# Optimization experiments

Hardware: AMD Instinct MI355X
Metric: run time of the kernel (lower is better)

The kernel has to match this reference:

```python
import jax, jax.numpy as jnp
import numpy as np

D_MODEL = 1024
N_HEADS = 16
D_K = D_MODEL // N_HEADS
B, T = 2, 2048


def setup_inputs() -> dict:
    key = jax.random.key(0)
    ks = jax.random.split(key, 12)
    s = 0.02
    return {
        "q": jax.random.normal(ks[0], (B, T, D_MODEL), jnp.float32),
        "k": jax.random.normal(ks[1], (B, T, D_MODEL), jnp.float32),
        "v": jax.random.normal(ks[2], (B, T, D_MODEL), jnp.float32),
        "Wq": jax.random.normal(ks[3], (D_MODEL, D_MODEL), jnp.float32) * s,
        "bq": jnp.zeros((D_MODEL,), jnp.float32),
        "Wk": jax.random.normal(ks[4], (D_MODEL, D_MODEL), jnp.float32) * s,
        "bk": jnp.zeros((D_MODEL,), jnp.float32),
        "Wv": jax.random.normal(ks[5], (D_MODEL, D_MODEL), jnp.float32) * s,
        "bv": jnp.zeros((D_MODEL,), jnp.float32),
        "Wo": jax.random.normal(ks[6], (D_MODEL, D_MODEL), jnp.float32) * s,
        "bo": jnp.zeros((D_MODEL,), jnp.float32),
        "mask": jnp.ones((B, T), jnp.int32),
        "causal": 1,
    }


def reference(q, k, v, Wq, bq, Wk, bk, Wv, bv, Wo, bo, mask, causal):
    Bq, Tq, D = q.shape
    Tk = k.shape[1]
    # projections (torch Linear: x @ W.T + b), split heads -> [B, H, T, d_k]
    qh = (q @ Wq.T + bq).reshape(Bq, Tq, N_HEADS, D_K).transpose(0, 2, 1, 3)
    kh = (k @ Wk.T + bk).reshape(Bq, Tk, N_HEADS, D_K).transpose(0, 2, 1, 3)
    vh = (v @ Wv.T + bv).reshape(Bq, Tk, N_HEADS, D_K).transpose(0, 2, 1, 3)
    scores = jnp.einsum("bhqd,bhkd->bhqk", qh, kh) / jnp.sqrt(jnp.float32(D_K))
    neg_inf = jnp.float32(-jnp.inf)
    if mask is not None:
        scores = jnp.where(mask[:, None, None, :] == 0, neg_inf, scores)
    if causal:
        causal_mask = jnp.tril(jnp.ones((Tq, Tq), jnp.float32))
        scores = jnp.where(causal_mask == 0, neg_inf, scores)
    attn = jax.nn.softmax(scores, axis=-1)
    out = jnp.einsum("bhqk,bhkd->bhqd", attn, vh)
    out = out.transpose(0, 2, 1, 3).reshape(Bq, Tq, D)
    return out @ Wo.T + bo
```

## Files before the change

kernel.cpp:

```cpp
#include <hip/hip_runtime.h>
#include <cstdint>
#include <cstddef>


typedef __bf16 bf16x8 __attribute__((ext_vector_type(8)));
typedef float f32x4 __attribute__((ext_vector_type(4)));

#define MFMA(a, b, c) __builtin_amdgcn_mfma_f32_16x16x32_bf16((a), (b), (c), 0, 0, 0)

static constexpr int D_MODEL = 1024;
static constexpr int T_ = 2048;
static constexpr int M_TOK = 4096;

__device__ __forceinline__ unsigned short f32_to_bf16(float f) {
    union { float f; uint32_t u; } v; v.f = f;
    uint32_t u = v.u;
    uint32_t r = u + 0x7fffu + ((u >> 16) & 1u);
    return (unsigned short)(r >> 16);
}
__device__ __forceinline__ unsigned f32_to_bf16_fast(float f) {
    union { float f; uint32_t u; } v; v.f = f;
    return (v.u + 0x8000u) >> 16;
}

typedef __attribute__((address_space(1))) void* as1_ptr;
typedef __attribute__((address_space(3))) void* as3_ptr;
__device__ __forceinline__ void gload_lds16(const void* g, void* l) {
    __builtin_amdgcn_global_load_lds((as1_ptr)(void*)g, (as3_ptr)l, 16, 0, 0);
}

__device__ __forceinline__ int keyperm(int k) {
    return (k & 32) | ((k & 12) << 1) | ((k & 16) >> 2) | (k & 3);
}

__global__ __launch_bounds__(256) void cvt_all(
    const float* __restrict__ q, const float* __restrict__ k,
    const float* __restrict__ v, const float* __restrict__ wq,
    const float* __restrict__ wk, const float* __restrict__ wv,
    const float* __restrict__ wo, ushort4* __restrict__ dst) {
    int i = blockIdx.x * blockDim.x + threadIdx.x;
    constexpr int R = 1 << 20;
    const float* s;
    int idx;
    if (i < 3 * R) {
        s = (i < R) ? q : (i < 2 * R) ? k : v;
        idx = i & (R - 1);
    } else {
        int j = i - 3 * R;
        int w = j >> 18;
        s = (w == 0) ? wq : (w == 1) ? wk : (w == 2) ? wv : wo;
        idx = j & ((1 << 18) - 1);
    }
    float4 f = ((const float4*)s)[idx];
    ushort4 o;
    o.x = (unsigned short)f32_to_bf16(f.x); o.y = (unsigned short)f32_to_bf16(f.y);
    o.z = (unsigned short)f32_to_bf16(f.z); o.w = (unsigned short)f32_to_bf16(f.w);
    dst[i] = o;
}

template<int MODE, int NT16>
__device__ __forceinline__ void gemm_body(
    const unsigned short* __restrict__ A, const unsigned short* __restrict__ W,
    const float* __restrict__ bias, void* __restrict__ outp,
    unsigned short* As, unsigned short* Ws, int bx, int by)
{
    constexpr bool SWAP = (MODE != 2);
    constexpr int BKE = 32;
    constexpr int ASZ = 128 * BKE;
    constexpr int WSZ = NT16 * 32 * BKE;
    constexpr int AL = ASZ / (256 * 8);
    constexpr int WL = WSZ / (256 * 8);
    constexpr int NKS = D_MODEL / BKE;
    const int tid = threadIdx.x;
    const int lane = tid & 63, wave = tid >> 6;
    const int wm = wave >> 1, wn = wave & 1;
    const int r16 = lane & 15, kg = lane >> 4;
    const int m_blk = by * 128, n_blk = bx * (NT16 * 32);

    const unsigned short* Ap[AL]; unsigned short* Albase[AL];
    #pragma unroll
    for (int j = 0; j < AL; ++j) {
        int si = j * 256 + tid;
        int row = si >> 2, p = si & 3, g = p ^ ((row >> 1) & 3);
        Ap[j] = A + (size_t)(m_blk + row) * D_MODEL + g * 8;
        Albase[j] = As + (j * 256 + wave * 64) * 8;
    }
    const unsigned short* Wp[WL]; unsigned short* Wlbase[WL];
    #pragma unroll
    for (int j = 0; j < WL; ++j) {
        int si = j * 256 + tid;
        int row = si >> 2, p = si & 3, g = p ^ ((row >> 1) & 3);
        Wp[j] = W + (size_t)(n_blk + row) * D_MODEL + g * 8;
        Wlbase[j] = Ws + (j * 256 + wave * 64) * 8;
    }

    int aoff[4], woff[NT16];
    #pragma unroll
    for (int mt = 0; mt < 4; ++mt) {
        int row = wm * 64 + mt * 16 + r16;
        aoff[mt] = row * BKE + ((kg ^ ((row >> 1) & 3)) * 8);
    }
    #pragma unroll
    for (int nt = 0; nt < NT16; ++nt) {
        int row = wn * (NT16 * 16) + nt * 16 + r16;
        woff[nt] = row * BKE + ((kg ^ ((row >> 1) & 3)) * 8);
    }

    f32x4 acc[4][NT16];
    #pragma unroll
    for (int mt = 0; mt < 4; ++mt)
        #pragma unroll
        for (int nt = 0; nt < NT16; ++nt) acc[mt][nt] = (f32x4){0, 0, 0, 0};

    auto stage = [&](int bb, int k0) {
        #pragma unroll
        for (int j = 0; j < AL; ++j)
            gload_lds16(Ap[j] + k0, Albase[j] + bb * ASZ);
        #pragma unroll
        for (int j = 0; j < WL; ++j)
            gload_lds16(Wp[j] + k0, Wlbase[j] + bb * WSZ);
    };

    stage(0, 0);
    stage(1, BKE);
    int cb = 0;
    for (int ks = 0; ks < NKS; ++ks) {
        if (ks + 1 < NKS) asm volatile("s_waitcnt vmcnt(4)" ::: "memory");
        else              asm volatile("s_waitcnt vmcnt(0)" ::: "memory");
        __builtin_amdgcn_s_barrier();
        __builtin_amdgcn_sched_barrier(0);
        if (ks + 2 < NKS) {
            int sb = cb + 2; if (sb >= 3) sb -= 3;
            stage(sb, (ks + 2) * BKE);
        }
        const unsigned short* Asb = As + cb * ASZ;
        const unsigned short* Wsb = Ws + cb * WSZ;
        bf16x8 af[4], wf[NT16];
        #pragma unroll
        for (int mt = 0; mt < 4; ++mt)
            af[mt] = *(const bf16x8*)(Asb + aoff[mt]);
        #pragma unroll
        for (int nt = 0; nt < NT16; ++nt)
            wf[nt] = *(const bf16x8*)(Wsb + woff[nt]);
        #pragma unroll
        for (int mt = 0; mt < 4; ++mt)
            #pragma unroll
            for (int nt = 0; nt < NT16; ++nt)
                acc[mt][nt] = SWAP ? MFMA(wf[nt], af[mt], acc[mt][nt])
                                   : MFMA(af[mt], wf[nt], acc[mt][nt]);
        cb = (cb == 2) ? 0 : cb + 1;
    }

    if (MODE == 2) {
        #pragma unroll
        for (int nt = 0; nt < NT16; ++nt) {
            int n = n_blk + wn * (NT16 * 16) + nt * 16 + r16;
            float bn = bias[n];
            int hh = n >> 6, dki = n & 63;
            #pragma unroll
            for (int mt = 0; mt < 4; ++mt) {
                int m0 = m_blk + wm * 64 + mt * 16 + kg * 4;
                int mp = (m0 & ~63) | keyperm(m0 & 63);
                int bb = mp >> 11, ti = mp & 2047;
                ushort4 pk;
                pk.x = f32_to_bf16(acc[mt][nt][0] + bn);
                pk.y = f32_to_bf16(acc[mt][nt][1] + bn);
                pk.z = f32_to_bf16(acc[mt][nt][2] + bn);
                pk.w = f32_to_bf16(acc[mt][nt][3] + bn);
                *(ushort4*)((unsigned short*)outp +
                    ((size_t)(bb * 16 + hh) * 64 + dki) * 2048 + ti) = pk;
            }
        }
    } else {
        #pragma unroll
        for (int nt = 0; nt < NT16; ++nt) {
            int n0 = n_blk + wn * (NT16 * 16) + nt * 16 + kg * 4;
            float4 bn4 = *(const float4*)(bias + n0);
            #pragma unroll
            for (int mt = 0; mt < 4; ++mt) {
                int m = m_blk + wm * 64 + mt * 16 + r16;
                if (MODE == 3) {
                    float4 st;
                    st.x = acc[mt][nt][0] + bn4.x; st.y = acc[mt][nt][1] + bn4.y;
                    st.z = acc[mt][nt][2] + bn4.z; st.w = acc[mt][nt][3] + bn4.w;
                    *(float4*)((float*)outp + (size_t)m * D_MODEL + n0) = st;
                } else {
                    ushort4 pk;
                    pk.x = f32_to_bf16(acc[mt][nt][0] + bn4.x);
                    pk.y = f32_to_bf16(acc[mt][nt][1] + bn4.y);
                    pk.z = f32_to_bf16(acc[mt][nt][2] + bn4.z);
                    pk.w = f32_to_bf16(acc[mt][nt][3] + bn4.w);
                    *(ushort4*)((unsigned short*)outp + (size_t)m * D_MODEL + n0) = pk;
                }
            }
        }
    }
}

__global__ __launch_bounds__(256) void gemm_qkv(
    const unsigned short* __restrict__ qb, const unsigned short* __restrict__ kb,
    const unsigned short* __restrict__ vb, const unsigned short* __restrict__ Wqb,
    const unsigned short* __restrict__ Wkb, const unsigned short* __restrict__ Wvb,
    const float* __restrict__ bq, const float* __restrict__ bk, const float* __restrict__ bv,
    unsigned short* __restrict__ Qhp, unsigned short* __restrict__ Khp,
    unsigned short* __restrict__ Vtp)
{
    __shared__ __align__(16) unsigned short As[3 * 128 * 32];
    __shared__ __align__(16) unsigned short Ws[3 * 128 * 32];
    int flat = blockIdx.x + (blockIdx.y << 3) + (blockIdx.z << 8);
    int w = (flat & 7) * 96 + (flat >> 3);
    int bx = w & 7, by = (w >> 3) & 31, z = w >> 8;
    const unsigned short* A = (z == 0) ? qb : (z == 1) ? kb : vb;
    const unsigned short* W = (z == 0) ? Wqb : (z == 1) ? Wkb : Wvb;
    const float* bias = (z == 0) ? bq : (z == 1) ? bk : bv;
    if (z < 2)
        gemm_body<0, 4>(A, W, bias, (z == 0) ? (void*)Qhp : (void*)Khp, As, Ws,
                        bx, by);
    else
        gemm_body<2, 4>(A, W, bias, (void*)Vtp, As, Ws, bx, by);
}

__global__ __launch_bounds__(256) void gemm_out(
    const unsigned short* __restrict__ ab, const unsigned short* __restrict__ Wob,
    const float* __restrict__ bo, float* __restrict__ outp)
{
    __shared__ __align__(16) unsigned short As[3 * 128 * 32];
    __shared__ __align__(16) unsigned short Ws[3 * 128 * 32];
    int flat = blockIdx.x + (blockIdx.y << 3);
    int w = (flat & 7) * 32 + (flat >> 3);
    int bx = w & 7, by = w >> 3;
    gemm_body<3, 4>(ab, Wob, bo, (void*)outp, As, Ws, bx, by);
}

__global__ __launch_bounds__(256) void attn_fwd(
    const unsigned short* __restrict__ Qh, const unsigned short* __restrict__ Kh,
    const unsigned short* __restrict__ Vt, const int* __restrict__ mask,
    const int* __restrict__ causal_p, unsigned short* __restrict__ attnout)
{
    __shared__ __align__(16) unsigned short Ks[2][64 * 64];
    __shared__ __align__(16) unsigned short Vs[2][64 * 64];
    __shared__ unsigned long long kmS[32];

    const int tid = threadIdx.x;
    const int lane = tid & 63, wave = tid >> 6;
    const int bh = blockIdx.x;
    const int y = blockIdx.y, y0 = y & 7, j4 = y >> 3;
    const int qc = (j4 == 0) ? y0 : (j4 == 1) ? (15 - y0)
                 : (j4 == 2) ? (16 + y0) : (31 - y0);
    const int b = bh >> 4, h = bh & 15;
    const int causal = *causal_p;
    const int r16 = lane & 15, kg = lane >> 4;

    const int q0 = qc * 64 + wave * 16;

    const unsigned short* Qb = Qh + (size_t)b * T_ * D_MODEL + h * 64;
    const unsigned short* Kb = Kh + (size_t)b * T_ * D_MODEL + h * 64;
    const unsigned short* Vb = Vt + (size_t)bh * 64 * T_;
    const int* mb = mask + b * T_;

    #pragma unroll
    for (int t = wave; t < 32; t += 4) {
        unsigned long long m = __ballot(mb[t * 64 + lane] != 0);
        if (lane == 0) kmS[t] = m;
    }

    bf16x8 qf0 = *(const bf16x8*)(Qb + (size_t)(q0 + r16) * D_MODEL + kg * 8);
    bf16x8 qf1 = *(const bf16x8*)(Qb + (size_t)(q0 + r16) * D_MODEL + 32 + kg * 8);

    float l = 0.f;
    f32x4 o[4];
    #pragma unroll
    for (int f = 0; f < 4; ++f) o[f] = (f32x4){0, 0, 0, 0};
    const float sc2 = 0.18033688011112042f;
    const int lim = wave * 16 + r16;

    const int nT = causal ? (qc + 1) : 32;

    auto stage = [&](int buf, int t) {
        int t0 = t * 64;
        #pragma unroll
        for (int j = 0; j < 2; ++j) {
            int si = j * 256 + tid;
            int row = si >> 3, cg = (si & 7) ^ (row & 7);
            gload_lds16(Kb + (size_t)(t0 + row) * D_MODEL + cg * 8,
                        (char*)Ks[buf] + (j * 256 + wave * 64) * 16);
            gload_lds16(Vb + (size_t)row * T_ + t0 + cg * 8,
                        (char*)Vs[buf] + (j * 256 + wave * 64) * 16);
        }
    };

    stage(0, 0);
    for (int t = 0; t < nT; ++t) {
        __syncthreads();
        if (t + 1 < nT) stage((t + 1) & 1, t + 1);
        const unsigned short* Kst = Ks[t & 1];
        const unsigned short* Vst = Vs[t & 1];
        const bool diag = causal && (t == qc);

        unsigned long long km = kmS[t];

        f32x4 s[4];
        #pragma unroll
        for (int c = 0; c < 4; ++c) {
            int key = c * 16 + r16;
            bf16x8 kf0 = *(const bf16x8*)(Kst + key * 64 + ((kg ^ (key & 7)) * 8));
            bf16x8 kf1 = *(const bf16x8*)(Kst + key * 64 + (((4 + kg) ^ (key & 7)) * 8));
            f32x4 z = (f32x4){0, 0, 0, 0};
            z = MFMA(kf0, qf0, z);
            z = MFMA(kf1, qf1, z);
            s[c] = z;
        }

        float pv[4][4];
        if (!diag && km == ~0ull) {
            #pragma unroll
            for (int c = 0; c < 4; ++c)
                #pragma unroll
                for (int r = 0; r < 4; ++r) {
                    float e = __builtin_amdgcn_exp2f(s[c][r] * sc2);
                    pv[c][r] = e; l += e;
                }
        } else {
            #pragma unroll
            for (int c = 0; c < 4; ++c) {
                unsigned mc = (unsigned)(km >> (c * 16));
                #pragma unroll
                for (int r = 0; r < 4; ++r) {
                    int kbit = kg * 4 + r;
                    bool ok = ((mc >> kbit) & 1) && (!diag || (c * 16 + kbit <= lim));
                    float e = ok ? __builtin_amdgcn_exp2f(s[c][r] * sc2) : 0.f;
                    pv[c][r] = e; l += e;
                }
            }
        }

        union pk_t { unsigned u[4]; bf16x8 v; };
        pk_t pa[2];
        #pragma unroll
        for (int c = 0; c < 4; ++c) {
            int half = (c & 1) * 2;
            pa[c >> 1].u[half]     = f32_to_bf16_fast(pv[c][0]) | (f32_to_bf16_fast(pv[c][1]) << 16);
            pa[c >> 1].u[half + 1] = f32_to_bf16_fast(pv[c][2]) | (f32_to_bf16_fast(pv[c][3]) << 16);
        }

        #pragma unroll
        for (int f = 0; f < 4; ++f) {
            int row = f * 16 + r16;
            int rx = row & 7;
            #pragma unroll
            for (int cp = 0; cp < 2; ++cp) {
                int g = cp * 4 + kg;
                bf16x8 vf = *(const bf16x8*)(Vst + row * 64 + ((g ^ rx) * 8));
                o[f] = MFMA(pa[cp].v, vf, o[f]);
            }
        }
    }

    l += __shfl_xor(l, 16, 64); l += __shfl_xor(l, 32, 64);
    float inv = (l > 0.f) ? 1.0f / l : 0.f;
    #pragma unroll
    for (int r = 0; r < 4; ++r) {
        int ql = kg * 4 + r;
        float iv = __shfl(inv, ql, 64);
        size_t base = ((size_t)(b * T_ + q0 + ql)) * D_MODEL + h * 64;
        #pragma unroll
        for (int f = 0; f < 4; ++f)
            attnout[base + f * 16 + r16] = f32_to_bf16(o[f][r] * iv);
    }
}

extern "C" void kernel_launch(void* const* d_in, const int* in_sizes, int n_in,
                              void* d_out, int out_size, void* d_ws, size_t ws_size,
                              hipStream_t stream) {
    const float* q  = (const float*)d_in[0];
    const float* k  = (const float*)d_in[1];
    const float* v  = (const float*)d_in[2];
    const float* Wq = (const float*)d_in[3];
    const float* bq = (const float*)d_in[4];
    const float* Wk = (const float*)d_in[5];
    const float* bk = (const float*)d_in[6];
    const float* Wv = (const float*)d_in[7];
    const float* bv = (const float*)d_in[8];
    const float* Wo = (const float*)d_in[9];
    const float* bo = (const float*)d_in[10];
    const int* mask   = (const int*)d_in[11];
    const int* causal = (const int*)d_in[12];

    const size_t SZ_TOK = (size_t)M_TOK * D_MODEL;
    const size_t SZ_W   = (size_t)D_MODEL * D_MODEL;

    unsigned short* qb  = (unsigned short*)d_ws;
    unsigned short* kb  = qb  + SZ_TOK;
    unsigned short* vb  = kb  + SZ_TOK;
    unsigned short* Wqb = vb  + SZ_TOK;
    unsigned short* Wkb = Wqb + SZ_W;
    unsigned short* Wvb = Wkb + SZ_W;
    unsigned short* Wob = Wvb + SZ_W;
    unsigned short* Qhp = Wob + SZ_W;
    unsigned short* Khp = Qhp + SZ_TOK;
    unsigned short* Vtp = Khp + SZ_TOK;
    unsigned short* ab  = Vtp + SZ_TOK;

    cvt_all<<<16384, 256, 0, stream>>>(q, k, v, Wq, Wk, Wv, Wo, (ushort4*)qb);

    gemm_qkv<<<dim3(D_MODEL / 128, M_TOK / 128, 3), 256, 0, stream>>>(
        qb, kb, vb, Wqb, Wkb, Wvb, bq, bk, bv, Qhp, Khp, Vtp);

    attn_fwd<<<dim3(32, 32), 256, 0, stream>>>(Qhp, Khp, Vtp, mask, causal, ab);

    gemm_out<<<dim3(D_MODEL / 128, M_TOK / 128), 256, 0, stream>>>(ab, Wob, bo,
                                                                   (float*)d_out);
}
```

Baseline: 220.8 us.

## Fold softmax scale into Q projection and compute row sums via MFMA

Applies the softmax scale (1/sqrt(dk)·log2e) in the Q projection epilogue, so the attention loop no longer multiplies every score before exp2. The softmax denominator is now built by MFMA against a ones vector, using the same bf16-rounded probabilities as the PV product, instead of scalar adds plus cross-lane shuffles. The change also precomputes K/V staging pointers, sets wave priority around the MFMA blocks and drops an unroll pragma. Rounding scaled Q to bf16 shifts numerics slightly, and the extra MFMAs add matrix-unit work.

```diff
diff --git a/kernel.cpp b/kernel.cpp
--- a/kernel.cpp
+++ b/kernel.cpp
@@ -62,7 +62,7 @@
 __device__ __forceinline__ void gemm_body(
     const unsigned short* __restrict__ A, const unsigned short* __restrict__ W,
     const float* __restrict__ bias, void* __restrict__ outp,
-    unsigned short* As, unsigned short* Ws, int bx, int by)
+    unsigned short* As, unsigned short* Ws, int bx, int by, float oscale)
 {
     constexpr bool SWAP = (MODE != 2);
     constexpr int BKE = 32;
@@ -163,10 +163,10 @@
                 int mp = (m0 & ~63) | keyperm(m0 & 63);
                 int bb = mp >> 11, ti = mp & 2047;
                 ushort4 pk;
-                pk.x = f32_to_bf16(acc[mt][nt][0] + bn);
-                pk.y = f32_to_bf16(acc[mt][nt][1] + bn);
-                pk.z = f32_to_bf16(acc[mt][nt][2] + bn);
-                pk.w = f32_to_bf16(acc[mt][nt][3] + bn);
+                pk.x = f32_to_bf16((acc[mt][nt][0] + bn) * oscale);
+                pk.y = f32_to_bf16((acc[mt][nt][1] + bn) * oscale);
+                pk.z = f32_to_bf16((acc[mt][nt][2] + bn) * oscale);
+                pk.w = f32_to_bf16((acc[mt][nt][3] + bn) * oscale);
                 *(ushort4*)((unsigned short*)outp +
                     ((size_t)(bb * 16 + hh) * 64 + dki) * 2048 + ti) = pk;
             }
@@ -181,15 +181,17 @@
                 int m = m_blk + wm * 64 + mt * 16 + r16;
                 if (MODE == 3) {
                     float4 st;
-                    st.x = acc[mt][nt][0] + bn4.x; st.y = acc[mt][nt][1] + bn4.y;
-                    st.z = acc[mt][nt][2] + bn4.z; st.w = acc[mt][nt][3] + bn4.w;
+                    st.x = (acc[mt][nt][0] + bn4.x) * oscale;
+                    st.y = (acc[mt][nt][1] + bn4.y) * oscale;
+                    st.z = (acc[mt][nt][2] + bn4.z) * oscale;
+                    st.w = (acc[mt][nt][3] + bn4.w) * oscale;
                     *(float4*)((float*)outp + (size_t)m * D_MODEL + n0) = st;
                 } else {
                     ushort4 pk;
-                    pk.x = f32_to_bf16(acc[mt][nt][0] + bn4.x);
-                    pk.y = f32_to_bf16(acc[mt][nt][1] + bn4.y);
-                    pk.z = f32_to_bf16(acc[mt][nt][2] + bn4.z);
-                    pk.w = f32_to_bf16(acc[mt][nt][3] + bn4.w);
+                    pk.x = f32_to_bf16((acc[mt][nt][0] + bn4.x) * oscale);
+                    pk.y = f32_to_bf16((acc[mt][nt][1] + bn4.y) * oscale);
+                    pk.z = f32_to_bf16((acc[mt][nt][2] + bn4.z) * oscale);
+                    pk.w = f32_to_bf16((acc[mt][nt][3] + bn4.w) * oscale);
                     *(ushort4*)((unsigned short*)outp + (size_t)m * D_MODEL + n0) = pk;
                 }
             }
@@ -213,11 +215,12 @@
     const unsigned short* A = (z == 0) ? qb : (z == 1) ? kb : vb;
     const unsigned short* W = (z == 0) ? Wqb : (z == 1) ? Wkb : Wvb;
     const float* bias = (z == 0) ? bq : (z == 1) ? bk : bv;
+    float osc = (z == 0) ? 0.18033688011112042f : 1.0f;
     if (z < 2)
         gemm_body<0, 4>(A, W, bias, (z == 0) ? (void*)Qhp : (void*)Khp, As, Ws,
-                        bx, by);
+                        bx, by, osc);
     else
-        gemm_body<2, 4>(A, W, bias, (void*)Vtp, As, Ws, bx, by);
+        gemm_body<2, 4>(A, W, bias, (void*)Vtp, As, Ws, bx, by, 1.0f);
 }
 
 __global__ __launch_bounds__(256) void gemm_out(
@@ -229,7 +232,7 @@
     int flat = blockIdx.x + (blockIdx.y << 3);
     int w = (flat & 7) * 32 + (flat >> 3);
     int bx = w & 7, by = w >> 3;
-    gemm_body<3, 4>(ab, Wob, bo, (void*)outp, As, Ws, bx, by);
+    gemm_body<3, 4>(ab, Wob, bo, (void*)outp, As, Ws, bx, by, 1.0f);
 }
 
 __global__ __launch_bounds__(256) void attn_fwd(
@@ -258,7 +261,6 @@
     const unsigned short* Vb = Vt + (size_t)bh * 64 * T_;
     const int* mb = mask + b * T_;
 
-    #pragma unroll
     for (int t = wave; t < 32; t += 4) {
         unsigned long long m = __ballot(mb[t * 64 + lane] != 0);
         if (lane == 0) kmS[t] = m;
@@ -267,25 +269,33 @@
     bf16x8 qf0 = *(const bf16x8*)(Qb + (size_t)(q0 + r16) * D_MODEL + kg * 8);
     bf16x8 qf1 = *(const bf16x8*)(Qb + (size_t)(q0 + r16) * D_MODEL + 32 + kg * 8);
 
-    float l = 0.f;
+    union { unsigned u[4]; bf16x8 v; } onef;
+    onef.u[0] = onef.u[1] = onef.u[2] = onef.u[3] = 0x3f803f80u;
+
+    f32x4 lacc = (f32x4){0, 0, 0, 0};
     f32x4 o[4];
     #pragma unroll
     for (int f = 0; f < 4; ++f) o[f] = (f32x4){0, 0, 0, 0};
-    const float sc2 = 0.18033688011112042f;
     const int lim = wave * 16 + r16;
 
     const int nT = causal ? (qc + 1) : 32;
 
+    const unsigned short* Kp[2]; const unsigned short* Vp[2];
+    char* Kl[2]; char* Vl[2];
+    #pragma unroll
+    for (int j = 0; j < 2; ++j) {
+        int si = j * 256 + tid;
+        int row = si >> 3, cg = (si & 7) ^ (row & 7);
+        Kp[j] = Kb + (size_t)row * D_MODEL + cg * 8;
+        Vp[j] = Vb + (size_t)row * T_ + cg * 8;
+        Kl[j] = (char*)Ks[0] + (j * 256 + wave * 64) * 16;
+        Vl[j] = (char*)Vs[0] + (j * 256 + wave * 64) * 16;
+    }
     auto stage = [&](int buf, int t) {
-        int t0 = t * 64;
         #pragma unroll
         for (int j = 0; j < 2; ++j) {
-            int si = j * 256 + tid;
-            int row = si >> 3, cg = (si & 7) ^ (row & 7);
-            gload_lds16(Kb + (size_t)(t0 + row) * D_MODEL + cg * 8,
-                        (char*)Ks[buf] + (j * 256 + wave * 64) * 16);
-            gload_lds16(Vb + (size_t)row * T_ + t0 + cg * 8,
-                        (char*)Vs[buf] + (j * 256 + wave * 64) * 16);
+            gload_lds16(Kp[j] + ((size_t)t << 16), Kl[j] + buf * 8192);
+            gload_lds16(Vp[j] + (t << 6),          Vl[j] + buf * 8192);
         }
     };
 
@@ -300,6 +310,7 @@
         unsigned long long km = kmS[t];
 
         f32x4 s[4];
+        __builtin_amdgcn_s_setprio(1);
         #pragma unroll
         for (int c = 0; c < 4; ++c) {
             int key = c * 16 + r16;
@@ -310,16 +321,15 @@
             z = MFMA(kf1, qf1, z);
             s[c] = z;
         }
+        __builtin_amdgcn_s_setprio(0);
 
         float pv[4][4];
         if (!diag && km == ~0ull) {
             #pragma unroll
             for (int c = 0; c < 4; ++c)
                 #pragma unroll
-                for (int r = 0; r < 4; ++r) {
-                    float e = __builtin_amdgcn_exp2f(s[c][r] * sc2);
-                    pv[c][r] = e; l += e;
-                }
+                for (int r = 0; r < 4; ++r)
+                    pv[c][r] = __builtin_amdgcn_exp2f(s[c][r]);
         } else {
             #pragma unroll
             for (int c = 0; c < 4; ++c) {
@@ -328,8 +338,7 @@
                 for (int r = 0; r < 4; ++r) {
                     int kbit = kg * 4 + r;
                     bool ok = ((mc >> kbit) & 1) && (!diag || (c * 16 + kbit <= lim));
-                    float e = ok ? __builtin_amdgcn_exp2f(s[c][r] * sc2) : 0.f;
-                    pv[c][r] = e; l += e;
+                    pv[c][r] = ok ? __builtin_amdgcn_exp2f(s[c][r]) : 0.f;
                 }
             }
         }
@@ -343,6 +352,9 @@
             pa[c >> 1].u[half + 1] = f32_to_bf16_fast(pv[c][2]) | (f32_to_bf16_fast(pv[c][3]) << 16);
         }
 
+        __builtin_amdgcn_s_setprio(1);
+        lacc = MFMA(pa[0].v, onef.v, lacc);
+        lacc = MFMA(pa[1].v, onef.v, lacc);
         #pragma unroll
         for (int f = 0; f < 4; ++f) {
             int row = f * 16 + r16;
@@ -354,15 +366,13 @@
                 o[f] = MFMA(pa[cp].v, vf, o[f]);
             }
         }
-    }
-
-    l += __shfl_xor(l, 16, 64); l += __shfl_xor(l, 32, 64);
-    float inv = (l > 0.f) ? 1.0f / l : 0.f;
+        __builtin_amdgcn_s_setprio(0);
+    }
+
     #pragma unroll
     for (int r = 0; r < 4; ++r) {
-        int ql = kg * 4 + r;
-        float iv = __shfl(inv, ql, 64);
-        size_t base = ((size_t)(b * T_ + q0 + ql)) * D_MODEL + h * 64;
+        float iv = (lacc[r] > 0.f) ? 1.0f / lacc[r] : 0.f;
+        size_t base = ((size_t)(b * T_ + q0 + kg * 4 + r)) * D_MODEL + h * 64;
         #pragma unroll
         for (int f = 0; f < 4; ++f)
             attnout[base + f * 16 + r16] = f32_to_bf16(o[f][r] * iv);
```

Result: no change. 218.9 us (-0.9%).
